# Kernel tuning notes

Hardware: AMD Instinct MI355X
Metric: run time of the kernel (lower is better)

## Reference

```python
import jax, jax.numpy as jnp
import numpy as np

B, N, C_IN, C_OUT, K, D_EMB = 32, 4096, 64, 64, 2, 16


def setup_inputs() -> dict:
    key = jax.random.key(0)
    ks = jax.random.split(key, 7)
    x = jax.random.normal(ks[0], (B, N, C_IN), jnp.float32)
    node_embeddings = jax.random.normal(ks[1], (N, D_EMB), jnp.float32)
    weights_pool = jax.random.normal(ks[2], (D_EMB, K, C_IN, C_OUT), jnp.float32) * 0.1
    bias_pool = jax.random.normal(ks[3], (D_EMB, C_OUT), jnp.float32) * 0.1
    lin_w = jax.random.normal(ks[4], (C_OUT, C_IN), jnp.float32) * 0.1
    lin_b = jax.random.normal(ks[5], (C_OUT,), jnp.float32) * 0.1
    adj = jax.random.uniform(ks[6], (N, N), jnp.float32)
    return dict(x=x, node_embeddings=node_embeddings, weights_pool=weights_pool,
                bias_pool=bias_pool, lin_w=lin_w, lin_b=lin_b, adj=adj)


def _sym_norm_adj(W):
    # W + 0.5*I, then D^{-1/2} W D^{-1/2} with D = diag(rowsum)
    n = W.shape[0]
    W = W + 0.5 * jnp.eye(n, dtype=W.dtype)
    sd = jnp.sqrt(1.0 / jnp.sum(W, axis=1))
    return sd[:, None] * W * sd[None, :]


def reference(x, node_embeddings, weights_pool, bias_pool, lin_w, lin_b, adj):
    n = node_embeddings.shape[0]
    # adaptive adjacency: softmax(relu(E E^T)) over neighbors
    supports_dyn = jax.nn.softmax(jax.nn.relu(node_embeddings @ node_embeddings.T), axis=1)
    supports = jnp.stack([jnp.eye(n, dtype=x.dtype), supports_dyn], axis=0)  # [K=2, N, N]
    # node-adaptive weights/bias generated from embeddings
    weights = jnp.einsum('nd,dkio->nkio', node_embeddings, weights_pool)  # [N,K,Cin,Cout]
    bias = node_embeddings @ bias_pool  # [N, Cout]
    # multi-hop aggregation + per-node conv
    x_g = jnp.einsum('knm,bmc->bnkc', supports, x)  # [B,N,K,Cin]
    x_gconv = jnp.einsum('bnki,nkio->bno', x_g, weights) + bias[None]  # [B,N,Cout]
    # static branch: init applies F.softmax(dim=1) to sym-normed adj, forward re-softmaxes dim=-1
    A = jax.nn.softmax(jax.nn.softmax(_sym_norm_adj(adj), axis=1), axis=-1)
    # einsum 'nm,bmc->bmc' == scale node m by sum_n A[n,m]
    scale = jnp.sum(A, axis=0)  # [N]
    x_static = (scale[None, :, None] * x) @ lin_w.T + lin_b  # [B,N,Cout]
    return x_gconv + jax.nn.sigmoid(x_static) * x_static
```

## Files before the change

### kernel.cpp

```cpp
#include <hip/hip_runtime.h>
#include <stdint.h>

#define Bdim 32
#define Ndim 4096
#define Cin  64
#define Cout 64
#define Demb 16

typedef __bf16 bf16x8 __attribute__((ext_vector_type(8)));
typedef float  f32x4  __attribute__((ext_vector_type(4)));

#define GLOBAL_AS(p) ((__attribute__((address_space(1))) void*)(p))
#define LDS_AS(p)    ((__attribute__((address_space(3))) void*)(p))
#define GLL(gp, lp)  __builtin_amdgcn_global_load_lds(GLOBAL_AS(gp), LDS_AS(lp), 16, 0, 0)

__device__ __forceinline__ uint16_t f2bf(float x) {
    union { float f; uint32_t u; } v; v.f = x;
    uint32_t r = v.u + 0x7FFFu + ((v.u >> 16) & 1u);
    return (uint16_t)(r >> 16);
}

__device__ __forceinline__ bf16x8 pack8(float4 a, float4 b) {
    union { uint16_t u[8]; bf16x8 v; } r;
    r.u[0] = f2bf(a.x); r.u[1] = f2bf(a.y); r.u[2] = f2bf(a.z); r.u[3] = f2bf(a.w);
    r.u[4] = f2bf(b.x); r.u[5] = f2bf(b.y); r.u[6] = f2bf(b.z); r.u[7] = f2bf(b.w);
    return r.v;
}

__global__ __launch_bounds__(256) void p1_prep(const float* __restrict__ E,
                                               const float* __restrict__ x,
                                               const float* __restrict__ adj,
                                               const float* __restrict__ pool,
                                               uint16_t* __restrict__ A,
                                               float* __restrict__ rs4,
                                               uint16_t* __restrict__ Xtt,
                                               float* __restrict__ sd,
                                               float* __restrict__ poolT) {
    __shared__ __align__(16) uint8_t smem[9232];
    const int t = threadIdx.x;
    const int blk = blockIdx.x;

    if (blk < 1024) {
        float* Er_s = (float*)smem;
        float* red_s = (float*)(smem + 1024);
        const int n0 = (blk >> 2) * 16;
        const int chunk = blk & 3;
        const int m0 = chunk * 1024;
        Er_s[t] = E[n0 * Demb + t];
        __syncthreads();
        for (int half = 0; half < 2; ++half) {
            float er[8][16];
#pragma unroll
            for (int r = 0; r < 8; ++r)
#pragma unroll
                for (int d = 0; d < 16; ++d) er[r][d] = Er_s[(half * 8 + r) * 16 + d];
            float sacc[8];
#pragma unroll
            for (int r = 0; r < 8; ++r) sacc[r] = 0.f;
            for (int c = 0; c < 4; ++c) {
                const int m = m0 + c * 256 + t;
                const float4* ep = (const float4*)(E + (size_t)m * Demb);
                float4 e0 = ep[0], e1 = ep[1], e2 = ep[2], e3 = ep[3];
                float em[16] = {e0.x, e0.y, e0.z, e0.w, e1.x, e1.y, e1.z, e1.w,
                                e2.x, e2.y, e2.z, e2.w, e3.x, e3.y, e3.z, e3.w};
#pragma unroll
                for (int r = 0; r < 8; ++r) {
                    float v = 0.f;
#pragma unroll
                    for (int d = 0; d < 16; ++d) v = fmaf(er[r][d], em[d], v);
                    v = fmaxf(v, 0.f);
                    const float e = __expf(v);
                    sacc[r] += e;
                    A[(size_t)(n0 + half * 8 + r) * Ndim + m] = f2bf(e);
                }
            }
#pragma unroll
            for (int r = 0; r < 8; ++r) {
                float s = sacc[r];
#pragma unroll
                for (int off = 32; off > 0; off >>= 1) s += __shfl_down(s, off, 64);
                __syncthreads();
                if ((t & 63) == 0) red_s[t >> 6] = s;
                __syncthreads();
                if (t == 0)
                    rs4[(size_t)(n0 + half * 8 + r) * 4 + chunk] =
                        red_s[0] + red_s[1] + red_s[2] + red_s[3];
            }
            __syncthreads();
        }
    } else if (blk < 3072) {
        auto T = (uint16_t(*)[72])smem;
        const int idx = blk - 1024;
        const int m0 = (idx & 63) * 64;
        const int b = idx >> 6;
        const int c = t & 63;
#pragma unroll
        for (int j = 0; j < 16; ++j) {
            const int m = (t >> 6) + j * 4;
            T[c][m] = f2bf(x[((size_t)b * Ndim + (m0 + m)) * Cin + c]);
        }
        __syncthreads();
        const int c2 = t >> 2, mo = (t & 3) * 16;
        const uint4* src = (const uint4*)&T[c2][mo];
        uint4 v0 = src[0], v1 = src[1];
        uint4* dst = (uint4*)(Xtt + (size_t)(b * Cin + c2) * Ndim + m0 + mo);
        dst[0] = v0;
        dst[1] = v1;
    } else if (blk < 7168) {
        float* red_s = (float*)smem;
        const int n = blk - 3072;
        const float4* ap = (const float4*)(adj + (size_t)n * Ndim);
        float s = 0.f;
#pragma unroll
        for (int q = 0; q < 4; ++q) {
            float4 a = ap[q * 256 + t];
            s += a.x + a.y + a.z + a.w;
        }
#pragma unroll
        for (int off = 32; off > 0; off >>= 1) s += __shfl_down(s, off, 64);
        if ((t & 63) == 0) red_s[t >> 6] = s;
        __syncthreads();
        if (t == 0) sd[n] = sqrtf(1.f / (red_s[0] + red_s[1] + red_s[2] + red_s[3] + 0.5f));
    } else {
        const int idx = blk - 7168;
        const int d = idx >> 2;
        const int base = (idx & 3) * 2048;
#pragma unroll
        for (int j = 0; j < 8; ++j) {
            const int e = base + j * 256 + t;
            const float v = pool[d * 8192 + e];
            poolT[d * 8192 + (e & 63) * 128 + (e >> 6)] = v;
        }
    }
}

__global__ __launch_bounds__(256) void p2_mid(const float* __restrict__ E,
                                              const float* __restrict__ adj,
                                              const float* __restrict__ sd,
                                              const float* __restrict__ poolT,
                                              const float* __restrict__ bias_pool,
                                              float* __restrict__ pscale,
                                              uint16_t* __restrict__ Wt,
                                              float* __restrict__ biasn,
                                              const float* __restrict__ rs4,
                                              float* __restrict__ invA) {
    __shared__ __align__(16) uint8_t smem[16384];
    const int t = threadIdx.x;
    const int blk = blockIdx.x;

    if (blk < 512) {
        float* cs = (float*)smem;
#pragma unroll
        for (int i = 0; i < 16; ++i) cs[i * 256 + t] = 0.f;
        __syncthreads();

        const int wv = t >> 6, l = t & 63;
        const int nb = blk * 8 + wv * 2;

        float sdm[64];
#pragma unroll
        for (int i = 0; i < 16; ++i) {
            float4 s4 = *(const float4*)(sd + i * 256 + l * 4);
            sdm[i * 4 + 0] = s4.x; sdm[i * 4 + 1] = s4.y;
            sdm[i * 4 + 2] = s4.z; sdm[i * 4 + 3] = s4.w;
        }
        float colsum[64];
#pragma unroll
        for (int k = 0; k < 64; ++k) colsum[k] = 0.f;

        for (int r = 0; r < 2; ++r) {
            const int n = nb + r;
            const float sdn = sd[n];
            float e1[64];
            float s1 = 0.f;
#pragma unroll
            for (int i = 0; i < 16; ++i) {
                float4 a4 = *(const float4*)(adj + (size_t)n * Ndim + i * 256 + l * 4);
                const int c0 = i * 256 + l * 4;
                float vv[4] = {a4.x, a4.y, a4.z, a4.w};
#pragma unroll
                for (int u = 0; u < 4; ++u) {
                    const float vd = vv[u] + ((c0 + u) == n ? 0.5f : 0.f);
                    const float e = __expf(sdn * vd * sdm[i * 4 + u]);
                    e1[i * 4 + u] = e;
                    s1 += e;
                }
            }
#pragma unroll
            for (int off = 32; off > 0; off >>= 1) s1 += __shfl_xor(s1, off, 64);
            const float inv1 = 1.f / s1;
            float s2 = 0.f;
#pragma unroll
            for (int k = 0; k < 64; ++k) {
                const float e = __expf(e1[k] * inv1);
                e1[k] = e;
                s2 += e;
            }
#pragma unroll
            for (int off = 32; off > 0; off >>= 1) s2 += __shfl_xor(s2, off, 64);
            const float inv2 = 1.f / s2;
#pragma unroll
            for (int k = 0; k < 64; ++k) colsum[k] = fmaf(e1[k], inv2, colsum[k]);
        }
#pragma unroll
        for (int k = 0; k < 64; ++k)
            atomicAdd(&cs[(k >> 2) * 256 + l * 4 + (k & 3)], colsum[k]);
        __syncthreads();
#pragma unroll
        for (int i = 0; i < 16; ++i)
            pscale[(size_t)blk * 4096 + i * 256 + t] = cs[i * 256 + t];
    } else if (blk < 1536) {
        float* En = (float*)smem;
        const int idx = blk - 512;
        const int ec = idx & 7;
        const int n0 = (idx >> 3) * 32;
        En[t] = E[n0 * Demb + t];
        En[t + 256] = E[n0 * Demb + t + 256];
        __syncthreads();

        const int e0 = ec * 1024 + t * 4;
        float4 P[16];
#pragma unroll
        for (int d = 0; d < 16; ++d) P[d] = *(const float4*)(poolT + d * 8192 + e0);

        for (int g = 0; g < 32; ++g) {
            float4 acc = {0.f, 0.f, 0.f, 0.f};
#pragma unroll
            for (int d = 0; d < 16; ++d) {
                const float e = En[g * 16 + d];
                acc.x = fmaf(e, P[d].x, acc.x);
                acc.y = fmaf(e, P[d].y, acc.y);
                acc.z = fmaf(e, P[d].z, acc.z);
                acc.w = fmaf(e, P[d].w, acc.w);
            }
            union { uint16_t u[4]; uint2 v; } r;
            r.u[0] = f2bf(acc.x); r.u[1] = f2bf(acc.y);
            r.u[2] = f2bf(acc.z); r.u[3] = f2bf(acc.w);
            *(uint2*)(Wt + (size_t)(n0 + g) * 8192 + e0) = r.v;
        }

        if (ec == 0) {
            const int o = t & 63, gq = t >> 6;
#pragma unroll
            for (int gi = 0; gi < 8; ++gi) {
                const int g = gi * 4 + gq;
                float a = 0.f;
#pragma unroll
                for (int d = 0; d < 16; ++d) a = fmaf(En[g * 16 + d], bias_pool[d * 64 + o], a);
                biasn[(size_t)(n0 + g) * 64 + o] = a;
            }
        }
    } else {
        const int n = (blk - 1536) * 256 + t;
        const float4 v = *(const float4*)(rs4 + (size_t)n * 4);
        invA[n] = 1.f / (v.x + v.y + v.z + v.w);
    }
}

#define GK 4096
#define GN 2048
#define K3_NT 64
__global__ __launch_bounds__(256) void k3_gemm(const uint16_t* __restrict__ Abf,
                                               const uint16_t* __restrict__ Bbf,
                                               const float* __restrict__ invA,
                                               uint16_t* __restrict__ Cbf) {
    __shared__ __align__(16) uint16_t As[2][128 * 64];
    __shared__ __align__(16) uint16_t Bs[2][128 * 64];
    const int t = threadIdx.x;
    const int lane = t & 63;
    const int wid = t >> 6;
    const int wr = wid >> 1;
    const int wc = wid & 1;

    const int bid = blockIdx.x;
    const int wgid = (bid & 7) * 64 + (bid >> 3);
    const int bm = (wgid >> 4) * 128;
    const int bn = (wgid & 15) * 128;

    const uint16_t* asrc[4];
    const uint16_t* bsrc[4];
    int cdst[4];
#pragma unroll
    for (int i = 0; i < 4; ++i) {
        const int c = t + i * 256;
        const int row = c >> 3, ch = c & 7;
        asrc[i] = Abf + (size_t)(bm + row) * GK + ((ch ^ (row & 7)) << 3);
        bsrc[i] = Bbf + (size_t)(bn + row) * GK + ((ch ^ (row & 7)) << 3);
        cdst[i] = c << 3;
    }

    int offA[4][2], offB[4][2];
#pragma unroll
    for (int f = 0; f < 4; ++f)
#pragma unroll
        for (int ks = 0; ks < 2; ++ks) {
            const int ra = wr * 64 + f * 16 + (lane & 15);
            offA[f][ks] = ra * 64 + (((ks * 4 + (lane >> 4)) ^ (ra & 7)) << 3);
            const int rb = wc * 64 + f * 16 + (lane & 15);
            offB[f][ks] = rb * 64 + (((ks * 4 + (lane >> 4)) ^ (rb & 7)) << 3);
        }

    f32x4 acc[4][4];
#pragma unroll
    for (int i = 0; i < 4; ++i)
#pragma unroll
        for (int j = 0; j < 4; ++j) acc[i][j] = (f32x4){0.f, 0.f, 0.f, 0.f};

#define K3_STAGE(buf, kt)                                  \
    do {                                                   \
        const size_t ko_ = (size_t)(kt) * 64;              \
        GLL(asrc[0] + ko_, &As[buf][cdst[0]]);             \
        GLL(asrc[1] + ko_, &As[buf][cdst[1]]);             \
        GLL(asrc[2] + ko_, &As[buf][cdst[2]]);             \
        GLL(asrc[3] + ko_, &As[buf][cdst[3]]);             \
        GLL(bsrc[0] + ko_, &Bs[buf][cdst[0]]);             \
        GLL(bsrc[1] + ko_, &Bs[buf][cdst[1]]);             \
        GLL(bsrc[2] + ko_, &Bs[buf][cdst[2]]);             \
        GLL(bsrc[3] + ko_, &Bs[buf][cdst[3]]);             \
    } while (0)

    K3_STAGE(0, 0);
    __syncthreads();

    for (int kt = 0; kt < K3_NT; ++kt) {
        const int cur = kt & 1;
        if (kt < K3_NT - 1) K3_STAGE(cur ^ 1, kt + 1);

        const uint16_t* Ab = As[cur];
        const uint16_t* Bb = Bs[cur];
        bf16x8 af[4][2], bfr[4][2];
#pragma unroll
        for (int ks = 0; ks < 2; ++ks) {
#pragma unroll
            for (int f = 0; f < 4; ++f) af[f][ks] = *(const bf16x8*)(Ab + offA[f][ks]);
#pragma unroll
            for (int j = 0; j < 4; ++j) bfr[j][ks] = *(const bf16x8*)(Bb + offB[j][ks]);
        }
        __builtin_amdgcn_s_setprio(1);
#pragma unroll
        for (int ks = 0; ks < 2; ++ks)
#pragma unroll
            for (int f = 0; f < 4; ++f)
#pragma unroll
                for (int j = 0; j < 4; ++j)
                    acc[f][j] = __builtin_amdgcn_mfma_f32_16x16x32_bf16(af[f][ks], bfr[j][ks], acc[f][j], 0, 0, 0);
        __builtin_amdgcn_s_setprio(0);
        __syncthreads();
    }
#undef K3_STAGE

#pragma unroll
    for (int f = 0; f < 4; ++f) {
        float invv[4];
#pragma unroll
        for (int r = 0; r < 4; ++r)
            invv[r] = invA[bm + wr * 64 + f * 16 + (lane >> 4) * 4 + r];
#pragma unroll
        for (int j = 0; j < 4; ++j)
#pragma unroll
            for (int r = 0; r < 4; ++r) {
                const int row = bm + wr * 64 + f * 16 + (lane >> 4) * 4 + r;
                const int col = bn + wc * 64 + j * 16 + (lane & 15);
                Cbf[(size_t)row * GN + col] = f2bf(acc[f][j][r] * invv[r]);
            }
    }
}

__global__ __launch_bounds__(256) void k6_gconv(const float* __restrict__ x,
                                                const uint16_t* __restrict__ XG,
                                                const uint16_t* __restrict__ Wt,
                                                const float* __restrict__ biasn,
                                                const float* __restrict__ pscale,
                                                const float* __restrict__ lin_w,
                                                const float* __restrict__ lin_b,
                                                float* __restrict__ out) {
    __shared__ __align__(16) uint16_t Lws[64][72];
    const int t = threadIdx.x;
    const int n0 = blockIdx.x * 4;
    const int w = t >> 6, lane = t & 63;
    const int n = n0 + w;

    float psum = 0.f;
#pragma unroll
    for (int k = 0; k < 8; ++k)
        psum += pscale[(size_t)(k * 64 + lane) * 4096 + n];

    {
        const int o = t >> 2, i0 = (t & 3) * 16;
        const float4* lp = (const float4*)(lin_w + o * 64 + i0);
        float4 a0 = lp[0], a1 = lp[1], a2 = lp[2], a3 = lp[3];
        union { uint16_t u[16]; uint4 v[2]; } r;
        r.u[0] = f2bf(a0.x); r.u[1] = f2bf(a0.y); r.u[2]  = f2bf(a0.z); r.u[3]  = f2bf(a0.w);
        r.u[4] = f2bf(a1.x); r.u[5] = f2bf(a1.y); r.u[6]  = f2bf(a1.z); r.u[7]  = f2bf(a1.w);
        r.u[8] = f2bf(a2.x); r.u[9] = f2bf(a2.y); r.u[10] = f2bf(a2.z); r.u[11] = f2bf(a2.w);
        r.u[12] = f2bf(a3.x); r.u[13] = f2bf(a3.y); r.u[14] = f2bf(a3.z); r.u[15] = f2bf(a3.w);
        *(uint4*)&Lws[o][i0] = r.v[0];
        *(uint4*)&Lws[o][i0 + 8] = r.v[1];
    }

    const int l15 = lane & 15;
    const int q8 = (lane >> 4) * 8;

    bf16x8 a[2][4];
#pragma unroll
    for (int mt = 0; mt < 2; ++mt) {
        const int b = mt * 16 + l15;
        const float* xp = x + ((size_t)b * Ndim + n) * 64 + q8;
        a[mt][0] = pack8(((const float4*)xp)[0], ((const float4*)xp)[1]);
        a[mt][1] = pack8(((const float4*)(xp + 32))[0], ((const float4*)(xp + 32))[1]);
        const uint16_t* gp = XG + (size_t)n * 2048 + b * 64 + q8;
        a[mt][2] = *(const bf16x8*)gp;
        a[mt][3] = *(const bf16x8*)(gp + 32);
    }

    f32x4 accg[2][4], accs[2][4];
#pragma unroll
    for (int mt = 0; mt < 2; ++mt)
#pragma unroll
        for (int j = 0; j < 4; ++j) {
            accg[mt][j] = (f32x4){0.f, 0.f, 0.f, 0.f};
            accs[mt][j] = (f32x4){0.f, 0.f, 0.f, 0.f};
        }

    const uint16_t* wp = Wt + (size_t)n * 8192 + l15 * 128 + q8;

    bf16x8 bw0[4], bw1[4];
#pragma unroll
    for (int j = 0; j < 4; ++j) bw0[j] = *(const bf16x8*)(wp + j * 2048);

    __syncthreads();

#pragma unroll
    for (int j = 0; j < 4; ++j) bw1[j] = *(const bf16x8*)(wp + j * 2048 + 32);
#pragma unroll
    for (int mt = 0; mt < 2; ++mt)
#pragma unroll
        for (int j = 0; j < 4; ++j)
            accg[mt][j] = __builtin_amdgcn_mfma_f32_16x16x32_bf16(a[mt][0], bw0[j], accg[mt][j], 0, 0, 0);
    {
        bf16x8 bl[4];
#pragma unroll
        for (int j = 0; j < 4; ++j) bl[j] = *(const bf16x8*)&Lws[j * 16 + l15][q8];
#pragma unroll
        for (int mt = 0; mt < 2; ++mt)
#pragma unroll
            for (int j = 0; j < 4; ++j)
                accs[mt][j] = __builtin_amdgcn_mfma_f32_16x16x32_bf16(a[mt][0], bl[j], accs[mt][j], 0, 0, 0);
    }
#pragma unroll
    for (int j = 0; j < 4; ++j) bw0[j] = *(const bf16x8*)(wp + j * 2048 + 64);
#pragma unroll
    for (int mt = 0; mt < 2; ++mt)
#pragma unroll
        for (int j = 0; j < 4; ++j)
            accg[mt][j] = __builtin_amdgcn_mfma_f32_16x16x32_bf16(a[mt][1], bw1[j], accg[mt][j], 0, 0, 0);
    {
        bf16x8 bl[4];
#pragma unroll
        for (int j = 0; j < 4; ++j) bl[j] = *(const bf16x8*)&Lws[j * 16 + l15][32 + q8];
#pragma unroll
        for (int mt = 0; mt < 2; ++mt)
#pragma unroll
            for (int j = 0; j < 4; ++j)
                accs[mt][j] = __builtin_amdgcn_mfma_f32_16x16x32_bf16(a[mt][1], bl[j], accs[mt][j], 0, 0, 0);
    }
#pragma unroll
    for (int j = 0; j < 4; ++j) bw1[j] = *(const bf16x8*)(wp + j * 2048 + 96);
#pragma unroll
    for (int mt = 0; mt < 2; ++mt)
#pragma unroll
        for (int j = 0; j < 4; ++j)
            accg[mt][j] = __builtin_amdgcn_mfma_f32_16x16x32_bf16(a[mt][2], bw0[j], accg[mt][j], 0, 0, 0);
#pragma unroll
    for (int mt = 0; mt < 2; ++mt)
#pragma unroll
        for (int j = 0; j < 4; ++j)
            accg[mt][j] = __builtin_amdgcn_mfma_f32_16x16x32_bf16(a[mt][3], bw1[j], accg[mt][j], 0, 0, 0);

#pragma unroll
    for (int off = 32; off > 0; off >>= 1) psum += __shfl_xor(psum, off, 64);
    const float sc = psum;

#pragma unroll
    for (int j = 0; j < 4; ++j) {
        const int o = j * 16 + l15;
        const float bn = biasn[(size_t)n * 64 + o];
        const float lb = lin_b[o];
#pragma unroll
        for (int mt = 0; mt < 2; ++mt)
#pragma unroll
            for (int r = 0; r < 4; ++r) {
                const int b = mt * 16 + (lane >> 4) * 4 + r;
                const float gg = accg[mt][j][r] + bn;
                const float xs = sc * accs[mt][j][r] + lb;
                out[((size_t)b * Ndim + n) * 64 + o] = gg + xs / (1.f + __expf(-xs));
            }
    }
}

extern "C" void kernel_launch(void* const* d_in, const int* in_sizes, int n_in,
                              void* d_out, int out_size, void* d_ws, size_t ws_size,
                              hipStream_t stream) {
    const float* x         = (const float*)d_in[0];
    const float* E         = (const float*)d_in[1];
    const float* pool      = (const float*)d_in[2];
    const float* bias_pool = (const float*)d_in[3];
    const float* lin_w     = (const float*)d_in[4];
    const float* lin_b     = (const float*)d_in[5];
    const float* adj       = (const float*)d_in[6];
    float* out = (float*)d_out;

    uint8_t* ws = (uint8_t*)d_ws;
    uint16_t* A      = (uint16_t*)(ws);
    uint16_t* Xtt    = (uint16_t*)(ws + 33554432);
    uint16_t* XG     = (uint16_t*)(ws + 50331648);
    uint16_t* Wt     = (uint16_t*)(ws + 67108864);
    float*    biasn  = (float*)   (ws + 134217728);
    float*    sd     = (float*)   (ws + 135266304);
    float*    poolT  = (float*)   (ws + 135299072);
    float*    invA   = (float*)   (ws + 135823360);
    float*    rs4    = (float*)   (ws + 135839744);
    float*    pscale = (float*)   (ws + 135905280);

    p1_prep<<<dim3(7232), dim3(256), 0, stream>>>(E, x, adj, pool, A, rs4, Xtt, sd, poolT);
    p2_mid<<<dim3(1552), dim3(256), 0, stream>>>(E, adj, sd, poolT, bias_pool, pscale, Wt, biasn, rs4, invA);
    k3_gemm<<<dim3(512), dim3(256), 0, stream>>>(A, Xtt, invA, XG);
    k6_gconv<<<dim3(1024), dim3(256), 0, stream>>>(x, XG, Wt, biasn, pscale, lin_w, lin_b, out);
}
```

Before: 380.9 us.

## Split each adjacency row across the whole block to cut registers and LDS atomics

The static-branch column-sum blocks now process one adjacency row at a time with all 256 threads, 16 columns per thread, instead of one wave per row with 64 columns per lane. Row softmax sums are combined through a small LDS reduction with block barriers. Each thread now owns its column accumulators for the block's 8 rows, so the LDS atomicAdd reduction is gone and results are written out directly as float4. This sharply lowers per-thread register use (from roughly 190 live floats) to raise occupancy and latency hiding on the 64 MB adjacency stream. The cost is two __syncthreads per row.

```diff
diff --git a/kernel.cpp b/kernel.cpp
--- a/kernel.cpp
+++ b/kernel.cpp
@@ -149,66 +149,71 @@
     const int blk = blockIdx.x;
 
     if (blk < 512) {
-        float* cs = (float*)smem;
-#pragma unroll
-        for (int i = 0; i < 16; ++i) cs[i * 256 + t] = 0.f;
-        __syncthreads();
-
-        const int wv = t >> 6, l = t & 63;
-        const int nb = blk * 8 + wv * 2;
-
-        float sdm[64];
-#pragma unroll
-        for (int i = 0; i < 16; ++i) {
-            float4 s4 = *(const float4*)(sd + i * 256 + l * 4);
-            sdm[i * 4 + 0] = s4.x; sdm[i * 4 + 1] = s4.y;
-            sdm[i * 4 + 2] = s4.z; sdm[i * 4 + 3] = s4.w;
-        }
-        float colsum[64];
-#pragma unroll
-        for (int k = 0; k < 64; ++k) colsum[k] = 0.f;
-
-        for (int r = 0; r < 2; ++r) {
+        float* red = (float*)smem;
+        const int w64 = t >> 6, lane = t & 63;
+        const int nb = blk * 8;
+        const int cbase = t * 4;
+
+        float sdm[4][4];
+#pragma unroll
+        for (int u = 0; u < 4; ++u) {
+            float4 s4 = *(const float4*)(sd + u * 1024 + cbase);
+            sdm[u][0] = s4.x; sdm[u][1] = s4.y; sdm[u][2] = s4.z; sdm[u][3] = s4.w;
+        }
+        float colacc[4][4];
+#pragma unroll
+        for (int u = 0; u < 4; ++u)
+#pragma unroll
+            for (int j = 0; j < 4; ++j) colacc[u][j] = 0.f;
+
+        for (int r = 0; r < 8; ++r) {
             const int n = nb + r;
             const float sdn = sd[n];
-            float e1[64];
+            float e1[4][4];
             float s1 = 0.f;
 #pragma unroll
-            for (int i = 0; i < 16; ++i) {
-                float4 a4 = *(const float4*)(adj + (size_t)n * Ndim + i * 256 + l * 4);
-                const int c0 = i * 256 + l * 4;
+            for (int u = 0; u < 4; ++u) {
+                float4 a4 = *(const float4*)(adj + (size_t)n * Ndim + u * 1024 + cbase);
                 float vv[4] = {a4.x, a4.y, a4.z, a4.w};
 #pragma unroll
-                for (int u = 0; u < 4; ++u) {
-                    const float vd = vv[u] + ((c0 + u) == n ? 0.5f : 0.f);
-                    const float e = __expf(sdn * vd * sdm[i * 4 + u]);
-                    e1[i * 4 + u] = e;
+                for (int j = 0; j < 4; ++j) {
+                    const float vd = vv[j] + ((u * 1024 + cbase + j) == n ? 0.5f : 0.f);
+                    const float e = __expf(sdn * vd * sdm[u][j]);
+                    e1[u][j] = e;
                     s1 += e;
                 }
             }
 #pragma unroll
             for (int off = 32; off > 0; off >>= 1) s1 += __shfl_xor(s1, off, 64);
-            const float inv1 = 1.f / s1;
+            if (lane == 0) red[w64] = s1;
+            __syncthreads();
+            const float inv1 = 1.f / (red[0] + red[1] + red[2] + red[3]);
+
             float s2 = 0.f;
 #pragma unroll
-            for (int k = 0; k < 64; ++k) {
-                const float e = __expf(e1[k] * inv1);
-                e1[k] = e;
-                s2 += e;
-            }
+            for (int u = 0; u < 4; ++u)
+#pragma unroll
+                for (int j = 0; j < 4; ++j) {
+                    const float e = __expf(e1[u][j] * inv1);
+                    e1[u][j] = e;
+                    s2 += e;
+                }
 #pragma unroll
             for (int off = 32; off > 0; off >>= 1) s2 += __shfl_xor(s2, off, 64);
-            const float inv2 = 1.f / s2;
-#pragma unroll
-            for (int k = 0; k < 64; ++k) colsum[k] = fmaf(e1[k], inv2, colsum[k]);
-        }
-#pragma unroll
-        for (int k = 0; k < 64; ++k)
-            atomicAdd(&cs[(k >> 2) * 256 + l * 4 + (k & 3)], colsum[k]);
-        __syncthreads();
-#pragma unroll
-        for (int i = 0; i < 16; ++i)
-            pscale[(size_t)blk * 4096 + i * 256 + t] = cs[i * 256 + t];
+            if (lane == 0) red[4 + w64] = s2;
+            __syncthreads();
+            const float inv2 = 1.f / (red[4] + red[5] + red[6] + red[7]);
+#pragma unroll
+            for (int u = 0; u < 4; ++u)
+#pragma unroll
+                for (int j = 0; j < 4; ++j)
+                    colacc[u][j] = fmaf(e1[u][j], inv2, colacc[u][j]);
+        }
+#pragma unroll
+        for (int u = 0; u < 4; ++u) {
+            float4 o = {colacc[u][0], colacc[u][1], colacc[u][2], colacc[u][3]};
+            *(float4*)(pscale + (size_t)blk * 4096 + u * 1024 + cbase) = o;
+        }
     } else if (blk < 1536) {
         float* En = (float*)smem;
         const int idx = blk - 512;
```

Measured after the change: 326.9 us. 1.17x faster.
